# Performance work log

Measured on AMD Instinct MI355X. Metric: run time of the kernel, lower is better.

Reference implementation:

```python
import jax, jax.numpy as jnp
import numpy as np

D = 256      # dim_model
H = 8        # n_head
FFN = 1024
L = 2        # n_layers
WIN = 100.0  # window_size of LocalisedEncoding
MINWL = 0.01 # min_wavelength of LocalisedEncoding
EPS = 1e-5


def _mass_sinusoid(mz):
    # depthcharge MassEncoder: min_wavelength=0.001, max_wavelength=10000
    n_sin = D // 2
    n_cos = D - n_sin
    base = 0.001 / (2.0 * np.pi)
    scale = 10000.0 / 0.001
    sin_term = (base * scale ** (np.arange(n_sin) / (n_sin - 1))).astype(np.float32)
    cos_term = (base * scale ** (np.arange(n_cos) / (n_cos - 1))).astype(np.float32)
    return jnp.concatenate([jnp.sin(mz / sin_term), jnp.cos(mz / cos_term)], axis=-1)


def _pe_lookup(pe, mass):
    # LocalisedEncoding.forward: clamp, linear index into precomputed table
    m = jnp.clip(mass, -WIN, WIN)
    idx = ((m + 1.0 + WIN) / MINWL).astype(jnp.int32)
    return pe[idx]


def _ln(x, g, b):
    mu = jnp.mean(x, axis=-1, keepdims=True)
    var = jnp.mean((x - mu) ** 2, axis=-1, keepdims=True)
    return (x - mu) * jax.lax.rsqrt(var + EPS) * g + b


def _forward(spectra, pe, latent, int_w, in_w, in_b, out_w, out_b,
             l1_w, l1_b, l2_w, l2_b, n1_g, n1_b, n2_g, n2_b):
    B, Np, _ = spectra.shape
    pad = jnp.sum(spectra, axis=2) == 0  # padded peaks
    # CustomPeakEncoder with mass=None, precursor_mass=None, dim_intensity=None
    peaks = _mass_sinusoid(spectra[:, :, :1]) + spectra[:, :, 1:2] @ int_w.T
    x = jnp.concatenate([jnp.broadcast_to(latent, (B, 1, D)), peaks], axis=1)
    mask = jnp.concatenate([jnp.zeros((B, 1), bool), pad], axis=1)  # [B,N]
    masses = jnp.concatenate([jnp.zeros((B, 1), spectra.dtype), spectra[:, :, 0]], axis=1)
    N = Np + 1
    hd = D // H
    scale = 1.0 / np.sqrt(hd)
    neg = jnp.asarray(-1e9, x.dtype)

    for l in range(L):
        wq, wk, wv = in_w[l, :D], in_w[l, D:2 * D], in_w[l, 2 * D:]
        bq, bk, bv = in_b[l, :D], in_b[l, D:2 * D], in_b[l, 2 * D:]
        if l == 0:
            # localized path: relative mass-difference encoding added to K/V
            pe0 = _pe_lookup(pe, jnp.zeros((), x.dtype))          # [D]
            q_in = x + pe0                                         # [B,N,D]
            rel = masses[:, None, :] - masses[:, :, None]          # m_j - m_i, [B,N,N]
            kv_in = x[:, None, :, :] + _pe_lookup(pe, rel)         # [B,N,N,D]
            Q = (q_in @ wq.T + bq).reshape(B, N, H, hd)
            K = (kv_in @ wk.T + bk).reshape(B, N, N, H, hd)
            V = (kv_in @ wv.T + bv).reshape(B, N, N, H, hd)
            s = jnp.einsum('bihd,bijhd->bhij', Q, K) * scale
            s = jnp.where(mask[:, None, None, :], neg, s)
            a = jax.nn.softmax(s, axis=-1)
            y = jnp.einsum('bhij,bijhd->bihd', a, V).reshape(B, N, D)
        else:
            Q = (x @ wq.T + bq).reshape(B, N, H, hd)
            K = (x @ wk.T + bk).reshape(B, N, H, hd)
            V = (x @ wv.T + bv).reshape(B, N, H, hd)
            s = jnp.einsum('bihd,bjhd->bhij', Q, K) * scale
            s = jnp.where(mask[:, None, None, :], neg, s)
            a = jax.nn.softmax(s, axis=-1)
            y = jnp.einsum('bhij,bjhd->bihd', a, V).reshape(B, N, D)
        y = y @ out_w[l].T + out_b[l]
        x = _ln(x + y, n1_g[l], n1_b[l])
        f = jax.nn.relu(x @ l1_w[l].T + l1_b[l]) @ l2_w[l].T + l2_b[l]
        x = _ln(x + f, n2_g[l], n2_b[l])
    return x


def setup_inputs() -> dict:
    key = jax.random.key(0)
    ks = jax.random.split(key, 14)
    B, Np = 16, 150
    mz = jax.random.uniform(ks[0], (B, Np, 1), dtype=jnp.float32) * 300.0
    inten = jax.random.uniform(ks[1], (B, Np, 1), dtype=jnp.float32)
    spectra = jnp.concatenate([mz, inten], axis=-1)
    # zero-pad the last 20 peaks of every other spectrum
    pad = (jnp.arange(Np)[None, :] >= 130) & (jnp.arange(B)[:, None] % 2 == 0)
    spectra = jnp.where(pad[:, :, None], 0.0, spectra)

    # LocalisedEncoding precomputed pe buffer (casanovo_style=True)
    max_len = int((WIN + 1) * 2 / MINWL)  # 20200
    pos = np.arange(max_len) - max_len // 2
    div = np.exp(np.arange(0, D, 2) * (-np.log(10000.0) / D))
    pe_np = np.zeros((max_len, D), np.float32)
    pe_np[:, : D // 2] = np.sin(pos[:, None] * div)
    pe_np[:, D // 2:] = np.cos(pos[:, None] * div)

    s = 0.05
    return {
        'spectra': spectra,
        'pe': jnp.asarray(pe_np),
        'latent': jax.random.normal(ks[2], (1, 1, D), jnp.float32) * s,
        'int_w': jax.random.normal(ks[3], (D, 1), jnp.float32) * s,
        'in_w': jax.random.normal(ks[4], (L, 3 * D, D), jnp.float32) * s,
        'in_b': jax.random.normal(ks[5], (L, 3 * D), jnp.float32) * s,
        'out_w': jax.random.normal(ks[6], (L, D, D), jnp.float32) * s,
        'out_b': jax.random.normal(ks[7], (L, D), jnp.float32) * s,
        'l1_w': jax.random.normal(ks[8], (L, FFN, D), jnp.float32) * s,
        'l1_b': jax.random.normal(ks[9], (L, FFN), jnp.float32) * s,
        'l2_w': jax.random.normal(ks[10], (L, D, FFN), jnp.float32) * s,
        'l2_b': jax.random.normal(ks[11], (L, D), jnp.float32) * s,
        'n1_g': jnp.ones((L, D), jnp.float32),
        'n1_b': jnp.zeros((L, D), jnp.float32),
        'n2_g': jnp.ones((L, D), jnp.float32),
        'n2_b': jnp.zeros((L, D), jnp.float32),
    }


def reference(spectra, pe, latent, int_w, in_w, in_b, out_w, out_b,
              l1_w, l1_b, l2_w, l2_b, n1_g, n1_b, n2_g, n2_b):
    return _forward(spectra, pe, latent, int_w, in_w, in_b, out_w, out_b,
                    l1_w, l1_b, l2_w, l2_b, n1_g, n1_b, n2_g, n2_b)
```

## Files before the change

### kernel.cpp

```cpp
#include <hip/hip_runtime.h>
#include <hip/hip_bf16.h>
#include <math.h>

#define BB 16
#define NP 150
#define NN 151
#define DD 256
#define HH 8
#define HD 32
#define FFN_ 1024
#define PE_LEN 20200
#define ROWS (BB*NN)
#define MPAD 2432
#define PE_PAD 20224


typedef __attribute__((ext_vector_type(8))) short short8;
typedef __attribute__((ext_vector_type(4))) float f32x4;
typedef __attribute__((ext_vector_type(4))) unsigned u32x4;

#if defined(__has_builtin)
#if __has_builtin(__builtin_amdgcn_fdot2_f32_bf16)
#define HAVE_DOT2 1
#endif
#endif
#ifndef HAVE_DOT2
#define HAVE_DOT2 0
#endif

__device__ __forceinline__ float r16(float x) {
    return __bfloat162float(__float2bfloat16(x));
}
__device__ __forceinline__ float us2f(unsigned short u) {
    return __uint_as_float((unsigned)u << 16);
}
__device__ __forceinline__ float lo2f(unsigned x) {
    return __uint_as_float(x << 16);
}
__device__ __forceinline__ float hi2f(unsigned x) {
    return __uint_as_float(x & 0xFFFF0000u);
}
__device__ __forceinline__ unsigned cvtpk(float lo, float hi) {
    unsigned r;
    asm("v_cvt_pk_bf16_f32 %0, %1, %2" : "=v"(r) : "v"(lo), "v"(hi));
    return r;
}
#if HAVE_DOT2
typedef __attribute__((ext_vector_type(2))) __bf16 bf16x2;
__device__ __forceinline__ float dot2bf(unsigned a, unsigned b, float acc) {
    bf16x2 av = __builtin_bit_cast(bf16x2, a);
    bf16x2 bv = __builtin_bit_cast(bf16x2, b);
    return __builtin_amdgcn_fdot2_f32_bf16(av, bv, acc, false);
}
#endif

#define PACK_BLOCKS 1024
__global__ __launch_bounds__(256) void buildpack_kernel(
    const float* __restrict__ spectra, const float* __restrict__ latent,
    const float* __restrict__ int_w, const float* __restrict__ pe,
    float* __restrict__ x, __hip_bfloat16* __restrict__ xb,
    __hip_bfloat16* __restrict__ xqb,
    float* __restrict__ masses, float* __restrict__ maskf,
    const float* __restrict__ in_w,  __hip_bfloat16* __restrict__ inw_p,
    const float* __restrict__ out_w, __hip_bfloat16* __restrict__ outw_p,
    const float* __restrict__ l1_w,  __hip_bfloat16* __restrict__ l1w_p,
    const float* __restrict__ l2_w,  __hip_bfloat16* __restrict__ l2w_p,
    __hip_bfloat16* __restrict__ pe_p)
{
    int tid = threadIdx.x;
    if (blockIdx.x < ROWS) {
        int bn = blockIdx.x;
        int b = bn / NN, n = bn % NN;
        float val;
        if (n == 0) {
            val = latent[tid];
            if (tid == 0) { masses[bn] = 0.0f; maskf[bn] = 0.0f; }
        } else {
            float mz = spectra[(b*NP + n - 1)*2 + 0];
            float it = spectra[(b*NP + n - 1)*2 + 1];
            int i = (tid < 128) ? tid : tid - 128;
            const double base_d = 0.001 / (2.0 * 3.141592653589793);
            double term_d = base_d * pow(1.0e7, (double)i / 127.0);
            float tf = (float)term_d;
            double arg = (double)mz / (double)tf;
            double sv = (tid < 128) ? sin(arg) : cos(arg);
            val = (float)sv + it * int_w[tid];
            if (tid == 0) {
                masses[bn] = mz;
                maskf[bn] = ((mz + it) == 0.0f) ? 1.0f : 0.0f;
            }
        }
        x[bn*DD + tid] = val;
        xb[bn*DD + tid] = __float2bfloat16(val);
        xqb[bn*DD + tid] = __float2bfloat16(val + pe[10100*DD + tid]);
    } else {
        long long base = (long long)(blockIdx.x - ROWS) * 256 + tid;
        const long long stride = (long long)PACK_BLOCKS * 256;
        for (long long i = base; i < (long long)PE_PAD*DD; i += stride)
            pe_p[i] = __float2bfloat16(i < (long long)PE_LEN*DD ? pe[i] : 0.0f);
        for (long long i = base; i < 2LL*768*DD; i += stride)
            inw_p[i] = __float2bfloat16(in_w[i]);
        for (long long i = base; i < 2LL*DD*DD; i += stride)
            outw_p[i] = __float2bfloat16(out_w[i]);
        for (long long i = base; i < 2LL*FFN_*DD; i += stride)
            l1w_p[i] = __float2bfloat16(l1_w[i]);
        for (long long i = base; i < 2LL*DD*FFN_; i += stride)
            l2w_p[i] = __float2bfloat16(l2_w[i]);
    }
}

template<typename CT>
__global__ __launch_bounds__(256) void gemm_mfma(
    const __hip_bfloat16* __restrict__ A, const __hip_bfloat16* __restrict__ W,
    const float* __restrict__ bias, CT* __restrict__ C,
    int M, int Nc, int K, int ldc, int relu)
{
    int wave = threadIdx.x >> 6;
    int lane = threadIdx.x & 63;
    int NT = Nc >> 5;
    int MT = (M + 31) >> 5;
    int id = blockIdx.x * 4 + wave;
    if (id >= MT * NT) return;
    int mt = id / NT, nt = id % NT;
    int m0 = mt * 32, n0 = nt * 32;
    int rl = lane & 15, q8 = (lane >> 4) * 8;

    const short8* Ap0 = (const short8*)(A + (size_t)(m0 + rl)*K + q8);
    const short8* Ap1 = (const short8*)(A + (size_t)(m0 + 16 + rl)*K + q8);
    const short8* Wp0 = (const short8*)(W + (size_t)(n0 + rl)*K + q8);
    const short8* Wp1 = (const short8*)(W + (size_t)(n0 + 16 + rl)*K + q8);

    f32x4 acc00 = {0,0,0,0}, acc01 = {0,0,0,0};
    f32x4 acc10 = {0,0,0,0}, acc11 = {0,0,0,0};
    int steps = K >> 5;
    for (int s = 0; s < steps; ++s) {
        short8 a0 = Ap0[s*4];
        short8 a1 = Ap1[s*4];
        short8 b0 = Wp0[s*4];
        short8 b1 = Wp1[s*4];
        acc00 = __builtin_amdgcn_mfma_f32_16x16x32_bf16(a0, b0, acc00, 0, 0, 0);
        acc01 = __builtin_amdgcn_mfma_f32_16x16x32_bf16(a0, b1, acc01, 0, 0, 0);
        acc10 = __builtin_amdgcn_mfma_f32_16x16x32_bf16(a1, b0, acc10, 0, 0, 0);
        acc11 = __builtin_amdgcn_mfma_f32_16x16x32_bf16(a1, b1, acc11, 0, 0, 0);
    }

    int rbase = (lane >> 4) * 4;
    #pragma unroll
    for (int sm = 0; sm < 2; ++sm) {
        #pragma unroll
        for (int sn = 0; sn < 2; ++sn) {
            f32x4 a = (sm == 0) ? (sn == 0 ? acc00 : acc01)
                                : (sn == 0 ? acc10 : acc11);
            int gc = n0 + sn*16 + rl;
            float bv = bias ? r16(bias[gc]) : 0.0f;
            #pragma unroll
            for (int rg = 0; rg < 4; ++rg) {
                int gr = m0 + sm*16 + rbase + rg;
                if (gr < M) {
                    float val = r16(a[rg]);
                    if (bias) val = r16(val + bv);
                    if (relu) val = fmaxf(val, 0.0f);
                    C[(size_t)gr*ldc + gc] = (CT)val;
                }
            }
        }
    }
}

__global__ __launch_bounds__(256) void gemm_pekv(
    const __hip_bfloat16* __restrict__ A, const __hip_bfloat16* __restrict__ W,
    __hip_bfloat16* __restrict__ C, int M, int Nc, int ldc)
{
    const int K = 256;
    int wave = threadIdx.x >> 6;
    int lane = threadIdx.x & 63;
    int NT = Nc >> 5;
    int MT4 = (M + 127) >> 7;
    int id = blockIdx.x * 4 + wave;
    if (id >= MT4 * NT) return;
    int mt = id / NT, nt = id % NT;
    int m0 = mt * 128, n0 = nt * 32;
    int rl = lane & 15, q8 = (lane >> 4) * 8;

    const short8* Ab = (const short8*)(A + (size_t)(m0 + rl)*K + q8);
    const short8* Wp0 = (const short8*)(W + (size_t)(n0 + rl)*K + q8);
    const short8* Wp1 = (const short8*)(W + (size_t)(n0 + 16 + rl)*K + q8);
    const int rstep = K >> 3;

    f32x4 acc[4][2][2] = {};
    for (int s = 0; s < 8; ++s) {
        short8 b0 = Wp0[s*4];
        short8 b1 = Wp1[s*4];
        short8 a[4][2];
        #pragma unroll
        for (int t = 0; t < 4; ++t) {
            a[t][0] = Ab[(size_t)(t*32)*rstep + s*4];
            a[t][1] = Ab[(size_t)(t*32+16)*rstep + s*4];
        }
        #pragma unroll
        for (int t = 0; t < 4; ++t) {
            acc[t][0][0] = __builtin_amdgcn_mfma_f32_16x16x32_bf16(a[t][0], b0, acc[t][0][0], 0, 0, 0);
            acc[t][0][1] = __builtin_amdgcn_mfma_f32_16x16x32_bf16(a[t][0], b1, acc[t][0][1], 0, 0, 0);
            acc[t][1][0] = __builtin_amdgcn_mfma_f32_16x16x32_bf16(a[t][1], b0, acc[t][1][0], 0, 0, 0);
            acc[t][1][1] = __builtin_amdgcn_mfma_f32_16x16x32_bf16(a[t][1], b1, acc[t][1][1], 0, 0, 0);
        }
    }

    int rbase = (lane >> 4) * 4;
    #pragma unroll
    for (int t = 0; t < 4; ++t) {
        #pragma unroll
        for (int sm = 0; sm < 2; ++sm) {
            #pragma unroll
            for (int sn = 0; sn < 2; ++sn) {
                f32x4 a = acc[t][sm][sn];
                int gc = n0 + sn*16 + rl;
                #pragma unroll
                for (int rg = 0; rg < 4; ++rg) {
                    int gr = m0 + t*32 + sm*16 + rbase + rg;
                    if (gr < M)
                        C[(size_t)gr*ldc + gc] = (__hip_bfloat16)r16(a[rg]);
                }
            }
        }
    }
}

__global__ __launch_bounds__(256) void gemm_qkv0(
    const __hip_bfloat16* __restrict__ xqb, const __hip_bfloat16* __restrict__ xb,
    const __hip_bfloat16* __restrict__ inw_p, const float* __restrict__ in_b,
    __hip_bfloat16* __restrict__ qb, __hip_bfloat16* __restrict__ kvb, int M)
{
    int wave = threadIdx.x >> 6;
    int lane = threadIdx.x & 63;
    int MT = (M + 31) >> 5;
    int id = blockIdx.x * 4 + wave;
    if (id >= MT * 24) return;
    int mt = id / 24, ntt = id % 24;
    bool isQ = (ntt < 8);
    const __hip_bfloat16* A = isQ ? xqb : xb;
    const __hip_bfloat16* W = inw_p + (isQ ? (size_t)ntt*32*DD
                                           : (size_t)(256 + (ntt-8)*32)*DD);
    const float* bias = in_b + (isQ ? ntt*32 : 256 + (ntt-8)*32);
    __hip_bfloat16* C = isQ ? qb : kvb;
    int ldc = isQ ? 256 : 512;
    int cbase = isQ ? ntt*32 : (ntt-8)*32;
    int m0 = mt * 32;
    int rl = lane & 15, q8 = (lane >> 4) * 8;
    const int K = DD;

    const short8* Ap0 = (const short8*)(A + (size_t)(m0 + rl)*K + q8);
    const short8* Ap1 = (const short8*)(A + (size_t)(m0 + 16 + rl)*K + q8);
    const short8* Wp0 = (const short8*)(W + (size_t)(rl)*K + q8);
    const short8* Wp1 = (const short8*)(W + (size_t)(16 + rl)*K + q8);

    f32x4 acc00 = {0,0,0,0}, acc01 = {0,0,0,0};
    f32x4 acc10 = {0,0,0,0}, acc11 = {0,0,0,0};
    for (int s = 0; s < K/32; ++s) {
        short8 a0 = Ap0[s*4];
        short8 a1 = Ap1[s*4];
        short8 b0 = Wp0[s*4];
        short8 b1 = Wp1[s*4];
        acc00 = __builtin_amdgcn_mfma_f32_16x16x32_bf16(a0, b0, acc00, 0, 0, 0);
        acc01 = __builtin_amdgcn_mfma_f32_16x16x32_bf16(a0, b1, acc01, 0, 0, 0);
        acc10 = __builtin_amdgcn_mfma_f32_16x16x32_bf16(a1, b0, acc10, 0, 0, 0);
        acc11 = __builtin_amdgcn_mfma_f32_16x16x32_bf16(a1, b1, acc11, 0, 0, 0);
    }

    int rbase = (lane >> 4) * 4;
    #pragma unroll
    for (int sm = 0; sm < 2; ++sm) {
        #pragma unroll
        for (int sn = 0; sn < 2; ++sn) {
            f32x4 a = (sm == 0) ? (sn == 0 ? acc00 : acc01)
                                : (sn == 0 ? acc10 : acc11);
            int gc = cbase + sn*16 + rl;
            float bv = r16(bias[sn*16 + rl]);
            #pragma unroll
            for (int rg = 0; rg < 4; ++rg) {
                int gr = m0 + sm*16 + rbase + rg;
                if (gr < M) {
                    float val = r16(a[rg]);
                    val = r16(val + bv);
                    C[(size_t)gr*ldc + gc] = (__hip_bfloat16)val;
                }
            }
        }
    }
}

template<bool USE_PE, int QS, int KS, int VS>
__global__ __launch_bounds__(256) void attn_kernel(
    const __hip_bfloat16* __restrict__ qp,
    const __hip_bfloat16* __restrict__ kp,
    const __hip_bfloat16* __restrict__ vp,
    const __hip_bfloat16* __restrict__ pekv,
    const float* __restrict__ masses, const float* __restrict__ maskf,
    __hip_bfloat16* __restrict__ yb)
{
    int b = blockIdx.x & 15;
    int i = blockIdx.x >> 4;
    int tid = threadIdx.x;
    int c = tid & 31;
    int g = tid >> 5;
    int h = c >> 2;

    __shared__ float sc[HH][152];
    __shared__ float msh[152];
    __shared__ int   tj[152];
    __shared__ __align__(16) float part[8][264];

    if (tid < NN) {
        msh[tid] = maskf[b*NN + tid];
        if (USE_PE) {
            double m = (double)masses[b*NN + tid] - (double)masses[b*NN + i];
            m = fmin(fmax(m, -100.0), 100.0);
            tj[tid] = (int)(((m + 1.0) + 100.0) / 0.01);
        }
    }

    unsigned qw[4];
    {
        const u32x4 q4 = *(const u32x4*)((const unsigned short*)qp
                            + (size_t)(b*NN + i)*QS + c*8);
        qw[0] = q4[0]; qw[1] = q4[1]; qw[2] = q4[2]; qw[3] = q4[3];
    }
#if !HAVE_DOT2
    float qf[8];
    #pragma unroll
    for (int w = 0; w < 4; ++w) { qf[2*w] = lo2f(qw[w]); qf[2*w+1] = hi2f(qw[w]); }
#endif
    __syncthreads();

    const float scale = 0.17677669529663687f;
    const unsigned short* kbase = (const unsigned short*)kp + (size_t)(b*NN)*KS + c*8;
    const unsigned short* vbase = (const unsigned short*)vp + (size_t)(b*NN)*VS + c*8;
    const unsigned short* pkb = (const unsigned short*)pekv + c*8;
    const unsigned short* pvb = (const unsigned short*)pekv + 256 + c*8;

    {
        int j = g;
        u32x4 kcur = *(const u32x4*)(kbase + (size_t)j*KS);
        u32x4 pcur;
        if (USE_PE) pcur = *(const u32x4*)(pkb + (size_t)tj[j]*512);
        for (int p = 0; p < 19; ++p) {
            int jn = j + 8;
            bool more = (jn < NN);
            u32x4 kn, pn;
            if (more) {
                kn = *(const u32x4*)(kbase + (size_t)jn*KS);
                if (USE_PE) pn = *(const u32x4*)(pkb + (size_t)tj[jn]*512);
            }
            float acc = 0.0f;
#if HAVE_DOT2
            #pragma unroll
            for (int w = 0; w < 4; ++w) {
                unsigned kd = kcur[w];
                if (USE_PE) {
                    unsigned pd = pcur[w];
                    float s0 = lo2f(kd) + lo2f(pd);
                    float s1 = hi2f(kd) + hi2f(pd);
                    kd = cvtpk(s0, s1);
                }
                acc = dot2bf(qw[w], kd, acc);
            }
#else
            #pragma unroll
            for (int w = 0; w < 4; ++w) {
                unsigned kd = kcur[w];
                float k0 = lo2f(kd), k1 = hi2f(kd);
                if (USE_PE) {
                    unsigned pd = pcur[w];
                    k0 = r16(k0 + lo2f(pd));
                    k1 = r16(k1 + hi2f(pd));
                }
                acc = fmaf(qf[2*w], k0, acc);
                acc = fmaf(qf[2*w+1], k1, acc);
            }
#endif
            acc += __shfl_xor(acc, 1);
            acc += __shfl_xor(acc, 2);
            if ((c & 3) == 0) {
                float s = acc * scale;
                if (msh[j] != 0.0f) s = -1e9f;
                sc[h][j] = s;
            }
            if (!more) break;
            j = jn; kcur = kn;
            if (USE_PE) pcur = pn;
        }
    }
    __syncthreads();

    {
        int lane = tid & 31;
        int hh = g;
        float mx = -INFINITY;
        for (int j = lane; j < NN; j += 32) mx = fmaxf(mx, sc[hh][j]);
        #pragma unroll
        for (int off = 16; off; off >>= 1) mx = fmaxf(mx, __shfl_xor(mx, off, 32));
        float sum = 0.0f;
        for (int j = lane; j < NN; j += 32) {
            float e = expf(sc[hh][j] - mx);
            sc[hh][j] = e;
            sum += e;
        }
        #pragma unroll
        for (int off = 16; off; off >>= 1) sum += __shfl_xor(sum, off, 32);
        float inv = 1.0f / sum;
        for (int j = lane; j < NN; j += 32) sc[hh][j] = r16(sc[hh][j] * inv);
    }
    __syncthreads();

    {
        float ya[8];
        #pragma unroll
        for (int u = 0; u < 8; ++u) ya[u] = 0.0f;

#if HAVE_DOT2
        u32x4 vA = *(const u32x4*)(vbase + (size_t)g*VS);
        u32x4 vB = *(const u32x4*)(vbase + (size_t)(g+8)*VS);
        u32x4 pA, pB;
        if (USE_PE) {
            pA = *(const u32x4*)(pvb + (size_t)tj[g]*512);
            pB = *(const u32x4*)(pvb + (size_t)tj[g+8]*512);
        }
        for (int t = 0; t < 9; ++t) {
            int jA = g + t*16, jB = jA + 8;
            u32x4 nvA, nvB, npA, npB;
            if (t < 8) {
                int nA = jA + 16, nB = jB + 16;
                nvA = *(const u32x4*)(vbase + (size_t)nA*VS);
                nvB = *(const u32x4*)(vbase + (size_t)nB*VS);
                if (USE_PE) {
                    npA = *(const u32x4*)(pvb + (size_t)tj[nA]*512);
                    npB = *(const u32x4*)(pvb + (size_t)tj[nB]*512);
                }
            }
            unsigned apair = cvtpk(sc[h][jA], sc[h][jB]);
            #pragma unroll
            for (int w = 0; w < 4; ++w) {
                unsigned lopair, hipair;
                if (USE_PE) {
                    float sA0 = lo2f(vA[w]) + lo2f(pA[w]);
                    float sA1 = hi2f(vA[w]) + hi2f(pA[w]);
                    float sB0 = lo2f(vB[w]) + lo2f(pB[w]);
                    float sB1 = hi2f(vB[w]) + hi2f(pB[w]);
                    lopair = cvtpk(sA0, sB0);
                    hipair = cvtpk(sA1, sB1);
                } else {
                    lopair = __builtin_amdgcn_perm(vB[w], vA[w], 0x05040100u);
                    hipair = __builtin_amdgcn_perm(vB[w], vA[w], 0x07060302u);
                }
                ya[2*w]   = dot2bf(apair, lopair, ya[2*w]);
                ya[2*w+1] = dot2bf(apair, hipair, ya[2*w+1]);
            }
            if (t < 8) {
                vA = nvA; vB = nvB;
                if (USE_PE) { pA = npA; pB = npB; }
            }
        }
        if (g + 144 < NN) {
            int jT = g + 144;
            u32x4 v = *(const u32x4*)(vbase + (size_t)jT*VS);
            u32x4 pq;
            if (USE_PE) pq = *(const u32x4*)(pvb + (size_t)tj[jT]*512);
            float aT = sc[h][jT];
            #pragma unroll
            for (int w = 0; w < 4; ++w) {
                float v0 = lo2f(v[w]), v1 = hi2f(v[w]);
                if (USE_PE) {
                    unsigned pk2 = cvtpk(v0 + lo2f(pq[w]), v1 + hi2f(pq[w]));
                    v0 = lo2f(pk2); v1 = hi2f(pk2);
                }
                ya[2*w]   = fmaf(aT, v0, ya[2*w]);
                ya[2*w+1] = fmaf(aT, v1, ya[2*w+1]);
            }
        }
#else
        int j = g;
        u32x4 vcur = *(const u32x4*)(vbase + (size_t)j*VS);
        u32x4 pcur;
        if (USE_PE) pcur = *(const u32x4*)(pvb + (size_t)tj[j]*512);
        float acur = sc[h][j];
        for (int p = 0; p < 19; ++p) {
            int jn = j + 8;
            bool more = (jn < NN);
            u32x4 vn, pn;
            float an = 0.0f;
            if (more) {
                vn = *(const u32x4*)(vbase + (size_t)jn*VS);
                if (USE_PE) pn = *(const u32x4*)(pvb + (size_t)tj[jn]*512);
                an = sc[h][jn];
            }
            #pragma unroll
            for (int w = 0; w < 4; ++w) {
                float v0 = lo2f(vcur[w]), v1 = hi2f(vcur[w]);
                if (USE_PE) {
                    v0 = r16(v0 + lo2f(pcur[w]));
                    v1 = r16(v1 + hi2f(pcur[w]));
                }
                ya[2*w]   = fmaf(acur, v0, ya[2*w]);
                ya[2*w+1] = fmaf(acur, v1, ya[2*w+1]);
            }
            if (!more) break;
            j = jn; vcur = vn; acur = an;
            if (USE_PE) pcur = pn;
        }
#endif
        f32x4* pp = (f32x4*)&part[g][c*8];
        pp[0] = f32x4{ya[0], ya[1], ya[2], ya[3]};
        pp[1] = f32x4{ya[4], ya[5], ya[6], ya[7]};
    }
    __syncthreads();

    {
        float s = part[0][tid];
        #pragma unroll
        for (int g2 = 1; g2 < 8; ++g2) s += part[g2][tid];
        yb[(size_t)(b*NN + i)*DD + tid] = __float2bfloat16(s);
    }
}

template<bool WRITE_B>
__global__ __launch_bounds__(256) void add_ln_kernel(
    const float* __restrict__ xin, const float* __restrict__ res,
    const float* __restrict__ g, const float* __restrict__ bb,
    float* __restrict__ xout, __hip_bfloat16* __restrict__ xbout)
{
    int r = blockIdx.x; int tid = threadIdx.x;
    float v = xin[r*DD + tid] + res[r*DD + tid];
    __shared__ float red[4];
    float s = v;
    #pragma unroll
    for (int off = 32; off; off >>= 1) s += __shfl_xor(s, off);
    if ((tid & 63) == 0) red[tid >> 6] = s;
    __syncthreads();
    float mu = (red[0] + red[1] + red[2] + red[3]) * (1.0f/256.0f);
    __syncthreads();
    float d = v - mu;
    float s2 = d*d;
    #pragma unroll
    for (int off = 32; off; off >>= 1) s2 += __shfl_xor(s2, off);
    if ((tid & 63) == 0) red[tid >> 6] = s2;
    __syncthreads();
    float var = (red[0] + red[1] + red[2] + red[3]) * (1.0f/256.0f);
    float out = d * (1.0f / sqrtf(var + 1e-5f)) * g[tid] + bb[tid];
    xout[r*DD + tid] = out;
    if (WRITE_B) xbout[r*DD + tid] = __float2bfloat16(out);
}

extern "C" void kernel_launch(void* const* d_in, const int* in_sizes, int n_in,
                              void* d_out, int out_size, void* d_ws, size_t ws_size,
                              hipStream_t stream)
{
    const float* spectra = (const float*)d_in[0];
    const float* pe      = (const float*)d_in[1];
    const float* latent  = (const float*)d_in[2];
    const float* int_w   = (const float*)d_in[3];
    const float* in_w    = (const float*)d_in[4];
    const float* in_b    = (const float*)d_in[5];
    const float* out_w   = (const float*)d_in[6];
    const float* out_b   = (const float*)d_in[7];
    const float* l1_w    = (const float*)d_in[8];
    const float* l1_b    = (const float*)d_in[9];
    const float* l2_w    = (const float*)d_in[10];
    const float* l2_b    = (const float*)d_in[11];
    const float* n1_g    = (const float*)d_in[12];
    const float* n1_b    = (const float*)d_in[13];
    const float* n2_g    = (const float*)d_in[14];
    const float* n2_b    = (const float*)d_in[15];

    float* x      = (float*)d_ws;
    float* y2     = x      + ROWS*DD;
    float* masses = y2     + ROWS*DD;
    float* maskf  = masses + ROWS;
    __hip_bfloat16* bp = (__hip_bfloat16*)(maskf + ROWS);
    __hip_bfloat16* xb    = bp;  bp += (size_t)MPAD*DD;
    __hip_bfloat16* xqb   = bp;  bp += (size_t)MPAD*DD;
    __hip_bfloat16* qb    = bp;  bp += (size_t)MPAD*DD;
    __hip_bfloat16* kvb   = bp;  bp += (size_t)MPAD*768;
    __hip_bfloat16* yb    = bp;  bp += (size_t)MPAD*DD;
    __hip_bfloat16* f1b   = bp;  bp += (size_t)MPAD*FFN_;
    __hip_bfloat16* pekv  = bp;  bp += (size_t)PE_PAD*512;
    __hip_bfloat16* pe_p  = bp;  bp += (size_t)PE_PAD*DD;
    __hip_bfloat16* inw_p = bp;  bp += (size_t)2*768*DD;
    __hip_bfloat16* outw_p= bp;  bp += (size_t)2*DD*DD;
    __hip_bfloat16* l1w_p = bp;  bp += (size_t)2*FFN_*DD;
    __hip_bfloat16* l2w_p = bp;  bp += (size_t)2*DD*FFN_;

    dim3 blk(256);
    auto GG = [](int M, int Nc){ return dim3((unsigned)((((M+31)>>5)*(Nc>>5) + 3) / 4)); };
    const unsigned STRIPS = (ROWS + 31) / 32;

    buildpack_kernel<<<ROWS + PACK_BLOCKS, blk, 0, stream>>>(
        spectra, latent, int_w, pe, x, xb, xqb, masses, maskf,
        in_w, inw_p, out_w, outw_p, l1_w, l1w_p, l2_w, l2w_p, pe_p);

    {
        unsigned mt4 = (PE_LEN + 127) >> 7;
        unsigned tiles = mt4 * (512 >> 5);
        gemm_pekv<<<dim3((tiles + 3) / 4), blk, 0, stream>>>(
            pe_p, inw_p + 256*DD, pekv, PE_LEN, 512, 512);
    }

    gemm_qkv0<<<dim3((STRIPS*24 + 3)/4), blk, 0, stream>>>(
        xqb, xb, inw_p, in_b, qb, kvb, ROWS);
    attn_kernel<true,256,512,512><<<ROWS, blk, 0, stream>>>(
        qb, kvb, kvb + 256, pekv, masses, maskf, yb);
    gemm_mfma<float><<<GG(ROWS, 256), blk, 0, stream>>>(
        yb, outw_p, out_b, y2, ROWS, 256, 256, 256, 0);
    add_ln_kernel<true><<<ROWS, blk, 0, stream>>>(x, y2, n1_g, n1_b, x, xb);
    gemm_mfma<__hip_bfloat16><<<GG(ROWS, 1024), blk, 0, stream>>>(
        xb, l1w_p, l1_b, f1b, ROWS, 1024, 256, 1024, 1);
    gemm_mfma<float><<<GG(ROWS, 256), blk, 0, stream>>>(
        f1b, l2w_p, l2_b, y2, ROWS, 256, 1024, 256, 0);
    add_ln_kernel<true><<<ROWS, blk, 0, stream>>>(x, y2, n2_g, n2_b, x, xb);

    gemm_mfma<__hip_bfloat16><<<GG(ROWS, 768), blk, 0, stream>>>(
        xb, inw_p + 768*DD, in_b + 768, kvb, ROWS, 768, 256, 768, 0);
    attn_kernel<false,768,768,768><<<ROWS, blk, 0, stream>>>(
        kvb, kvb + 256, kvb + 512, nullptr, masses, maskf, yb);
    gemm_mfma<float><<<GG(ROWS, 256), blk, 0, stream>>>(
        yb, outw_p + 256*DD, out_b + 256, y2, ROWS, 256, 256, 256, 0);
    add_ln_kernel<true><<<ROWS, blk, 0, stream>>>(x, y2, n1_g + 256, n1_b + 256, x, xb);
    gemm_mfma<__hip_bfloat16><<<GG(ROWS, 1024), blk, 0, stream>>>(
        xb, l1w_p + FFN_*DD, l1_b + 1024, f1b, ROWS, 1024, 256, 1024, 1);
    gemm_mfma<float><<<GG(ROWS, 256), blk, 0, stream>>>(
        f1b, l2w_p + DD*FFN_, l2_b + 256, y2, ROWS, 256, 1024, 256, 0);
    add_ln_kernel<false><<<ROWS, blk, 0, stream>>>(x, y2, n2_g + 256, n2_b + 256,
                                                   (float*)d_out, nullptr);
}
```

Measured before the change: 316.7 us.

## Split-K skinny GEMM for N=256 projections and merge PE-KV with QKV0 launch

Adds a split-K MFMA kernel for the N=256 output projections and FFN down-projections. Each block computes a 16x32 tile, its four waves each take a quarter of K, and the partial sums are reduced through shared memory before bias is added. This replaces a grid of about 152 blocks with 1208 blocks so more of the CUs are busy. Separately, the PE-KV table GEMM and the layer-0 QKV GEMM are fused into one launch that dispatches by block index, removing a launch and letting the two overlap. The costs are a shared-memory reduction with a barrier and a change in fp32 summation order.

New measurement: 304.0 us. -4.0%, faster.

```diff
diff --git a/kernel.cpp b/kernel.cpp
--- a/kernel.cpp
+++ b/kernel.cpp
@@ -167,22 +167,76 @@
     }
 }
 
-__global__ __launch_bounds__(256) void gemm_pekv(
+template<int K>
+__global__ __launch_bounds__(256) void gemm_skinny(
     const __hip_bfloat16* __restrict__ A, const __hip_bfloat16* __restrict__ W,
-    __hip_bfloat16* __restrict__ C, int M, int Nc, int ldc)
-{
-    const int K = 256;
+    const float* __restrict__ bias, float* __restrict__ C,
+    int M, int Nc, int ldc)
+{
+    int NT = Nc >> 5;
+    int id = blockIdx.x;
+    int mt = id / NT, nt = id % NT;
+    int m0 = mt * 16, n0 = nt * 32;
     int wave = threadIdx.x >> 6;
     int lane = threadIdx.x & 63;
+    int rl = lane & 15, q8 = (lane >> 4) * 8;
+    const int K4 = K >> 2;
+    int k0 = wave * K4;
+
+    const short8* Ap  = (const short8*)(A + (size_t)(m0 + rl)*K + k0 + q8);
+    const short8* Wp0 = (const short8*)(W + (size_t)(n0 + rl)*K + k0 + q8);
+    const short8* Wp1 = (const short8*)(W + (size_t)(n0 + 16 + rl)*K + k0 + q8);
+
+    f32x4 acc0 = {0,0,0,0}, acc1 = {0,0,0,0};
+    #pragma unroll
+    for (int s = 0; s < K4/32; ++s) {
+        short8 a  = Ap[s*4];
+        short8 b0 = Wp0[s*4];
+        short8 b1 = Wp1[s*4];
+        acc0 = __builtin_amdgcn_mfma_f32_16x16x32_bf16(a, b0, acc0, 0, 0, 0);
+        acc1 = __builtin_amdgcn_mfma_f32_16x16x32_bf16(a, b1, acc1, 0, 0, 0);
+    }
+
+    __shared__ float red[4][8][65];
+    #pragma unroll
+    for (int rg = 0; rg < 4; ++rg) {
+        red[wave][rg][lane]   = acc0[rg];
+        red[wave][4+rg][lane] = acc1[rg];
+    }
+    __syncthreads();
+
+    #pragma unroll
+    for (int t = 0; t < 2; ++t) {
+        int sl = wave*2 + t;
+        float s = red[0][sl][lane] + red[1][sl][lane]
+                + red[2][sl][lane] + red[3][sl][lane];
+        int rg = sl & 3, sn = sl >> 2;
+        int gr = m0 + (lane >> 4)*4 + rg;
+        int gc = n0 + sn*16 + rl;
+        float val = r16(s);
+        val = r16(val + r16(bias[gc]));
+        if (gr < M) C[(size_t)gr*ldc + gc] = val;
+    }
+}
+
+#define PEKV_BLK 632u
+#define QKV0_BLK 456u
+
+__device__ __forceinline__ void pekv_body(
+    unsigned bid, int wave, int lane,
+    const __hip_bfloat16* __restrict__ A, const __hip_bfloat16* __restrict__ W,
+    __hip_bfloat16* __restrict__ C)
+{
+    const int K = 256, Nc = 512, ldc = 512, M = PE_LEN;
     int NT = Nc >> 5;
     int MT4 = (M + 127) >> 7;
-    int id = blockIdx.x * 4 + wave;
+    int id = bid * 4 + wave;
     if (id >= MT4 * NT) return;
     int mt = id / NT, nt = id % NT;
     int m0 = mt * 128, n0 = nt * 32;
     int rl = lane & 15, q8 = (lane >> 4) * 8;
 
-    const short8* Ab = (const short8*)(A + (size_t)(m0 + rl)*K + q8);
+    const short8* Ab  = (const short8*)(A + (size_t)(m0 + rl)*K + q8);
     const short8* Wp0 = (const short8*)(W + (size_t)(n0 + rl)*K + q8);
     const short8* Wp1 = (const short8*)(W + (size_t)(n0 + 16 + rl)*K + q8);
     const int rstep = K >> 3;
@@ -226,15 +280,14 @@
     }
 }
 
-__global__ __launch_bounds__(256) void gemm_qkv0(
+__device__ __forceinline__ void qkv0_body(
+    unsigned bid, int wave, int lane,
     const __hip_bfloat16* __restrict__ xqb, const __hip_bfloat16* __restrict__ xb,
     const __hip_bfloat16* __restrict__ inw_p, const float* __restrict__ in_b,
     __hip_bfloat16* __restrict__ qb, __hip_bfloat16* __restrict__ kvb, int M)
 {
-    int wave = threadIdx.x >> 6;
-    int lane = threadIdx.x & 63;
     int MT = (M + 31) >> 5;
-    int id = blockIdx.x * 4 + wave;
+    int id = bid * 4 + wave;
     if (id >= MT * 24) return;
     int mt = id / 24, ntt = id % 24;
     bool isQ = (ntt < 8);
@@ -287,6 +340,22 @@
             }
         }
     }
+}
+
+__global__ __launch_bounds__(256) void pekv_qkv0_kernel(
+    const __hip_bfloat16* __restrict__ pe_p, const __hip_bfloat16* __restrict__ wkv0,
+    __hip_bfloat16* __restrict__ pekv,
+    const __hip_bfloat16* __restrict__ xqb, const __hip_bfloat16* __restrict__ xb,
+    const __hip_bfloat16* __restrict__ inw_p, const float* __restrict__ in_b,
+    __hip_bfloat16* __restrict__ qb, __hip_bfloat16* __restrict__ kvb)
+{
+    int wave = threadIdx.x >> 6;
+    int lane = threadIdx.x & 63;
+    if (blockIdx.x < PEKV_BLK)
+        pekv_body(blockIdx.x, wave, lane, pe_p, wkv0, pekv);
+    else
+        qkv0_body(blockIdx.x - PEKV_BLK, wave, lane, xqb, xb, inw_p, in_b,
+                  qb, kvb, ROWS);
 }
 
 template<bool USE_PE, int QS, int KS, int VS>
@@ -591,43 +660,37 @@
 
     dim3 blk(256);
     auto GG = [](int M, int Nc){ return dim3((unsigned)((((M+31)>>5)*(Nc>>5) + 3) / 4)); };
-    const unsigned STRIPS = (ROWS + 31) / 32;
+    const unsigned SKINNY = (ROWS/16) * (256 >> 5);
 
     buildpack_kernel<<<ROWS + PACK_BLOCKS, blk, 0, stream>>>(
         spectra, latent, int_w, pe, x, xb, xqb, masses, maskf,
         in_w, inw_p, out_w, outw_p, l1_w, l1w_p, l2_w, l2w_p, pe_p);
 
-    {
-        unsigned mt4 = (PE_LEN + 127) >> 7;
-        unsigned tiles = mt4 * (512 >> 5);
-        gemm_pekv<<<dim3((tiles + 3) / 4), blk, 0, stream>>>(
-            pe_p, inw_p + 256*DD, pekv, PE_LEN, 512, 512);
-    }
-
-    gemm_qkv0<<<dim3((STRIPS*24 + 3)/4), blk, 0, stream>>>(
-        xqb, xb, inw_p, in_b, qb, kvb, ROWS);
+    pekv_qkv0_kernel<<<PEKV_BLK + QKV0_BLK, blk, 0, stream>>>(
+        pe_p, inw_p + 256*DD, pekv, xqb, xb, inw_p, in_b, qb, kvb);
+
     attn_kernel<true,256,512,512><<<ROWS, blk, 0, stream>>>(
         qb, kvb, kvb + 256, pekv, masses, maskf, yb);
-    gemm_mfma<float><<<GG(ROWS, 256), blk, 0, stream>>>(
-        yb, outw_p, out_b, y2, ROWS, 256, 256, 256, 0);
+    gemm_skinny<256><<<SKINNY, blk, 0, stream>>>(
+        yb, outw_p, out_b, y2, ROWS, 256, 256);
     add_ln_kernel<true><<<ROWS, blk, 0, stream>>>(x, y2, n1_g, n1_b, x, xb);
     gemm_mfma<__hip_bfloat16><<<GG(ROWS, 1024), blk, 0, stream>>>(
         xb, l1w_p, l1_b, f1b, ROWS, 1024, 256, 1024, 1);
-    gemm_mfma<float><<<GG(ROWS, 256), blk, 0, stream>>>(
-        f1b, l2w_p, l2_b, y2, ROWS, 256, 1024, 256, 0);
+    gemm_skinny<1024><<<SKINNY, blk, 0, stream>>>(
+        f1b, l2w_p, l2_b, y2, ROWS, 256, 256);
     add_ln_kernel<true><<<ROWS, blk, 0, stream>>>(x, y2, n2_g, n2_b, x, xb);
 
     gemm_mfma<__hip_bfloat16><<<GG(ROWS, 768), blk, 0, stream>>>(
         xb, inw_p + 768*DD, in_b + 768, kvb, ROWS, 768, 256, 768, 0);
     attn_kernel<false,768,768,768><<<ROWS, blk, 0, stream>>>(
         kvb, kvb + 256, kvb + 512, nullptr, masses, maskf, yb);
-    gemm_mfma<float><<<GG(ROWS, 256), blk, 0, stream>>>(
-        yb, outw_p + 256*DD, out_b + 256, y2, ROWS, 256, 256, 256, 0);
+    gemm_skinny<256><<<SKINNY, blk, 0, stream>>>(
+        yb, outw_p + 256*DD, out_b + 256, y2, ROWS, 256, 256);
     add_ln_kernel<true><<<ROWS, blk, 0, stream>>>(x, y2, n1_g + 256, n1_b + 256, x, xb);
     gemm_mfma<__hip_bfloat16><<<GG(ROWS, 1024), blk, 0, stream>>>(
         xb, l1w_p + FFN_*DD, l1_b + 1024, f1b, ROWS, 1024, 256, 1024, 1);
-    gemm_mfma<float><<<GG(ROWS, 256), blk, 0, stream>>>(
-        f1b, l2w_p + DD*FFN_, l2_b + 256, y2, ROWS, 256, 1024, 256, 0);
+    gemm_skinny<1024><<<SKINNY, blk, 0, stream>>>(
+        f1b, l2w_p + DD*FFN_, l2_b + 256, y2, ROWS, 256, 256);
     add_ln_kernel<false><<<ROWS, blk, 0, stream>>>(x, y2, n2_g + 256, n2_b + 256,
                                                    (float*)d_out, nullptr);
 }
```
